# Optimization experiments

Hardware: AMD Instinct MI355X
Metric: run time of the kernel (lower is better)

## Reference

```python
import jax, jax.numpy as jnp
import numpy as np

EXP = 2          # self.exp
NEG = -1e9       # mask fill value
B, N1, DIM, F = 4, 1024, 1024, 4
N = N1 + 1
NTOT = F * N     # 4100


def _normalize(x):
    # L2-normalize along last dim; also return the norm (keepdims)
    n = jnp.sqrt(jnp.sum(x * x, axis=-1, keepdims=True))
    return x / n, n


def setup_inputs() -> dict:
    key = jax.random.key(0)
    k1, k2 = jax.random.split(key)
    lhs = jax.random.normal(k1, (B, N1, DIM), dtype=jnp.float32)
    rhs = jax.random.normal(k2, (B, NTOT, DIM), dtype=jnp.float32)
    return {"lhs": lhs, "rhs": rhs}


def reference(lhs, rhs):
    b, n1, dim = lhs.shape
    n = n1 + 1
    ntot = rhs.shape[1]
    f = ntot // n

    lhs_n, lhs_norm = _normalize(lhs)          # (B,N1,D), (B,N1,1)
    rhs_n, _ = _normalize(rhs)                 # (B,Ntot,D)

    # cosine similarity GEMM + power epilogue
    sim = jnp.einsum('bnd,bmd->bnm', lhs_n, rhs_n) ** EXP   # (B,N1,Ntot)

    # view as (B, N1, F, N); torch masks:
    #   sim4[..., -N1:][~eye] = -1e9   (off-diagonal of last N1 cols)
    #   sim4[..., 0] = -1e9            (first col of each frame)
    # net keep condition: j == i + 1
    sim4 = sim.reshape(b, n1, f, n)
    i = jnp.arange(n1)[:, None, None]   # (N1,1,1)
    j = jnp.arange(n)[None, None, :]    # (1,1,N)
    keep = (j == i + 1)                 # (N1,1,N), broadcasts over F
    sim4 = jnp.where(keep, sim4, jnp.float32(NEG))

    return sim4.reshape(b, n1, ntot), lhs_norm
```

## Files before the change

### kernel.cpp

```cpp
#include <hip/hip_runtime.h>

#define BB   4
#define N1   1024
#define DIM  1024
#define FF   4
#define NN   1025
#define NTOT (FF * NN)
#define SIM_TOTAL ((size_t)BB * N1 * NTOT)
#define NEGV (-1e9f)

typedef float f4 __attribute__((ext_vector_type(4)));

__device__ __forceinline__ f4 nt_load(const f4* p)  { return __builtin_nontemporal_load(p); }
__device__ __forceinline__ void nt_store(f4* p, f4 v) { __builtin_nontemporal_store(v, p); }

__global__ __launch_bounds__(256)
void lcs_kernel(const float* __restrict__ lhs,
                const float* __restrict__ rhs,
                float* __restrict__ out) {
    const int lane = threadIdx.x & 63;
    const int row  = (blockIdx.x << 2) | (threadIdx.x >> 6);
    const int b    = row >> 10;
    const int i    = row & (N1 - 1);

    f4* orow4 = (f4*)(out + (size_t)row * NTOT);
    const f4 negv = { NEGV, NEGV, NEGV, NEGV };
#pragma unroll
    for (int c = 0; c < 16; ++c)
        nt_store(orow4 + lane + 64 * c, negv);
    if (lane == 0)
        nt_store(orow4 + 1024, negv);

    const f4* lrow = (const f4*)(lhs + (size_t)row * DIM);
    f4 lv[4];
#pragma unroll
    for (int c = 0; c < 4; ++c)
        lv[c] = nt_load(lrow + lane + 64 * c);

    float l2 = 0.f;
#pragma unroll
    for (int c = 0; c < 4; ++c)
        l2 += lv[c].x * lv[c].x + lv[c].y * lv[c].y
            + lv[c].z * lv[c].z + lv[c].w * lv[c].w;

    float dot[FF], r2[FF];
#pragma unroll
    for (int f = 0; f < FF; ++f) {
        const size_t rrow_idx = (size_t)b * NTOT + (size_t)f * NN + (i + 1);
        const f4* rrow = (const f4*)(rhs + rrow_idx * DIM);
        float d = 0.f, r = 0.f;
#pragma unroll
        for (int c = 0; c < 4; ++c) {
            const f4 rv = nt_load(rrow + lane + 64 * c);
            d += lv[c].x * rv.x + lv[c].y * rv.y + lv[c].z * rv.z + lv[c].w * rv.w;
            r += rv.x * rv.x + rv.y * rv.y + rv.z * rv.z + rv.w * rv.w;
        }
        dot[f] = d;
        r2[f]  = r;
    }

    float vals[9];
    vals[0] = l2;
#pragma unroll
    for (int f = 0; f < FF; ++f) {
        vals[1 + 2 * f] = dot[f];
        vals[2 + 2 * f] = r2[f];
    }
#pragma unroll
    for (int q = 0; q < 9; ++q) {
#pragma unroll
        for (int off = 32; off > 0; off >>= 1)
            vals[q] += __shfl_xor(vals[q], off, 64);
    }

    asm volatile("s_waitcnt vmcnt(0)" ::: "memory");
    if (lane == 0) {
        const float l2s = vals[0];
        float* orow = out + (size_t)row * NTOT;
#pragma unroll
        for (int f = 0; f < FF; ++f) {
            const float d = vals[1 + 2 * f];
            const float r = vals[2 + 2 * f];
            orow[f * NN + i + 1] = (d * d) / (l2s * r);
        }
        out[SIM_TOTAL + row] = sqrtf(l2s);
    }
}

extern "C" void kernel_launch(void* const* d_in, const int* in_sizes, int n_in,
                              void* d_out, int out_size, void* d_ws, size_t ws_size,
                              hipStream_t stream) {
    const float* lhs = (const float*)d_in[0];
    const float* rhs = (const float*)d_in[1];
    float* out = (float*)d_out;

    lcs_kernel<<<BB * N1 / 4, 256, 0, stream>>>(lhs, rhs, out);
}
```

Baseline: 129.3 us.

## Process two rows per wave, prefetch all inputs, and write masked float4s directly

Each wave now handles two rows. All lhs and rhs vectors for both rows are loaded up front to raise memory-level parallelism. The -1e9 fill skips the float4 slots that hold diagonal values; the lane owning each such slot writes a full float4 that mixes the sim value with fill. This removes the scalar overwrite and its ordering wait. Nontemporal load/store hints are dropped, and launch bounds request 2 blocks per CU, which risks register pressure from the large prefetch arrays.

Result: no change. 129.0 us (-0.2%).

```diff
diff --git a/kernel.cpp b/kernel.cpp
--- a/kernel.cpp
+++ b/kernel.cpp
@@ -11,79 +11,114 @@
 
 typedef float f4 __attribute__((ext_vector_type(4)));
 
-__device__ __forceinline__ f4 nt_load(const f4* p)  { return __builtin_nontemporal_load(p); }
-__device__ __forceinline__ void nt_store(f4* p, f4 v) { __builtin_nontemporal_store(v, p); }
-
-__global__ __launch_bounds__(256)
+__global__ __launch_bounds__(256, 2)
 void lcs_kernel(const float* __restrict__ lhs,
                 const float* __restrict__ rhs,
                 float* __restrict__ out) {
     const int lane = threadIdx.x & 63;
-    const int row  = (blockIdx.x << 2) | (threadIdx.x >> 6);
-    const int b    = row >> 10;
-    const int i    = row & (N1 - 1);
+    const int w    = (blockIdx.x << 2) | (threadIdx.x >> 6);
 
-    f4* orow4 = (f4*)(out + (size_t)row * NTOT);
+    int rows[2];
+    rows[0] = w;
+    rows[1] = w + 2048;
+
+    f4 lv[2][4];
+    f4 rv[2][FF][4];
+#pragma unroll
+    for (int t = 0; t < 2; ++t) {
+        const int row = rows[t];
+        const int b   = row >> 10;
+        const int i   = row & (N1 - 1);
+        const f4* lrow = (const f4*)(lhs + (size_t)row * DIM);
+#pragma unroll
+        for (int c = 0; c < 4; ++c)
+            lv[t][c] = lrow[lane + 64 * c];
+#pragma unroll
+        for (int f = 0; f < FF; ++f) {
+            const f4* rrow =
+                (const f4*)(rhs + ((size_t)b * NTOT + (size_t)f * NN + (i + 1)) * DIM);
+#pragma unroll
+            for (int c = 0; c < 4; ++c)
+                rv[t][f][c] = rrow[lane + 64 * c];
+        }
+    }
+
+    int kf[2][FF], mf[2][FF];
+    unsigned smask[2];
+#pragma unroll
+    for (int t = 0; t < 2; ++t) {
+        const int i = rows[t] & (N1 - 1);
+        unsigned m = 0;
+#pragma unroll
+        for (int f = 0; f < FF; ++f) {
+            const int j = f * NN + i + 1;
+            kf[t][f] = j >> 2;
+            mf[t][f] = j & 3;
+            if ((kf[t][f] & 63) == lane)
+                m |= 1u << (kf[t][f] >> 6);
+        }
+        smask[t] = m;
+    }
+
     const f4 negv = { NEGV, NEGV, NEGV, NEGV };
 #pragma unroll
-    for (int c = 0; c < 16; ++c)
-        nt_store(orow4 + lane + 64 * c, negv);
-    if (lane == 0)
-        nt_store(orow4 + 1024, negv);
-
-    const f4* lrow = (const f4*)(lhs + (size_t)row * DIM);
-    f4 lv[4];
+    for (int t = 0; t < 2; ++t) {
+        f4* orow4 = (f4*)(out + (size_t)rows[t] * NTOT);
 #pragma unroll
-    for (int c = 0; c < 4; ++c)
-        lv[c] = nt_load(lrow + lane + 64 * c);
-
-    float l2 = 0.f;
-#pragma unroll
-    for (int c = 0; c < 4; ++c)
-        l2 += lv[c].x * lv[c].x + lv[c].y * lv[c].y
-            + lv[c].z * lv[c].z + lv[c].w * lv[c].w;
-
-    float dot[FF], r2[FF];
-#pragma unroll
-    for (int f = 0; f < FF; ++f) {
-        const size_t rrow_idx = (size_t)b * NTOT + (size_t)f * NN + (i + 1);
-        const f4* rrow = (const f4*)(rhs + rrow_idx * DIM);
-        float d = 0.f, r = 0.f;
-#pragma unroll
-        for (int c = 0; c < 4; ++c) {
-            const f4 rv = nt_load(rrow + lane + 64 * c);
-            d += lv[c].x * rv.x + lv[c].y * rv.y + lv[c].z * rv.z + lv[c].w * rv.w;
-            r += rv.x * rv.x + rv.y * rv.y + rv.z * rv.z + rv.w * rv.w;
-        }
-        dot[f] = d;
-        r2[f]  = r;
+        for (int c = 0; c < 16; ++c)
+            if (!((smask[t] >> c) & 1))
+                orow4[lane + 64 * c] = negv;
+        if (lane == 0 && !((smask[t] >> 16) & 1))
+            orow4[1024] = negv;
     }
 
-    float vals[9];
-    vals[0] = l2;
 #pragma unroll
-    for (int f = 0; f < FF; ++f) {
-        vals[1 + 2 * f] = dot[f];
-        vals[2 + 2 * f] = r2[f];
-    }
+    for (int t = 0; t < 2; ++t) {
+        float vals[9];
+        float l2 = 0.f;
 #pragma unroll
-    for (int q = 0; q < 9; ++q) {
-#pragma unroll
-        for (int off = 32; off > 0; off >>= 1)
-            vals[q] += __shfl_xor(vals[q], off, 64);
-    }
-
-    asm volatile("s_waitcnt vmcnt(0)" ::: "memory");
-    if (lane == 0) {
-        const float l2s = vals[0];
-        float* orow = out + (size_t)row * NTOT;
+        for (int c = 0; c < 4; ++c)
+            l2 += lv[t][c].x * lv[t][c].x + lv[t][c].y * lv[t][c].y
+                + lv[t][c].z * lv[t][c].z + lv[t][c].w * lv[t][c].w;
+        vals[0] = l2;
 #pragma unroll
         for (int f = 0; f < FF; ++f) {
-            const float d = vals[1 + 2 * f];
-            const float r = vals[2 + 2 * f];
-            orow[f * NN + i + 1] = (d * d) / (l2s * r);
+            float d = 0.f, r = 0.f;
+#pragma unroll
+            for (int c = 0; c < 4; ++c) {
+                const f4 a = lv[t][c], bz = rv[t][f][c];
+                d += a.x * bz.x + a.y * bz.y + a.z * bz.z + a.w * bz.w;
+                r += bz.x * bz.x + bz.y * bz.y + bz.z * bz.z + bz.w * bz.w;
+            }
+            vals[1 + 2 * f] = d;
+            vals[2 + 2 * f] = r;
         }
-        out[SIM_TOTAL + row] = sqrtf(l2s);
+
+#pragma unroll
+        for (int q = 0; q < 9; ++q) {
+#pragma unroll
+            for (int off = 32; off > 0; off >>= 1)
+                vals[q] += __shfl_xor(vals[q], off, 64);
+        }
+
+        const float l2s = vals[0];
+        f4* orow4 = (f4*)(out + (size_t)rows[t] * NTOT);
+#pragma unroll
+        for (int f = 0; f < FF; ++f) {
+            if ((kf[t][f] & 63) == lane) {
+                const float d   = vals[1 + 2 * f];
+                const float r   = vals[2 + 2 * f];
+                const float sim = (d * d) / (l2s * r);
+                f4 v;
+                v.x = (mf[t][f] == 0) ? sim : NEGV;
+                v.y = (mf[t][f] == 1) ? sim : NEGV;
+                v.z = (mf[t][f] == 2) ? sim : NEGV;
+                v.w = (mf[t][f] == 3) ? sim : NEGV;
+                orow4[kf[t][f]] = v;
+            }
+        }
+        if (lane == 0)
+            out[SIM_TOTAL + rows[t]] = sqrtf(l2s);
     }
 }
 
@@ -94,5 +129,5 @@
     const float* rhs = (const float*)d_in[1];
     float* out = (float*)d_out;
 
-    lcs_kernel<<<BB * N1 / 4, 256, 0, stream>>>(lhs, rhs, out);
+    lcs_kernel<<<512, 256, 0, stream>>>(lhs, rhs, out);
 }
```

## Hoist all input loads, skip overwritten fill stores, drop nontemporal hints

Applied to the files above, without the earlier changes.

Issues all lhs and rhs vector loads up front so they are in flight together, before the -1e9 fill stores. Each lane works out which float4 slots hold a diagonal similarity value, skips the fill store for those slots, and later writes the full float4 with the sim value merged in. This removes the duplicate store and the vmcnt(0) wait. Nontemporal load/store builtins are replaced with ordinary accesses, which changes cache behaviour for a write-heavy kernel, and holding the prefetched rhs rows raises register use.

New measurement: 126.3 us. 1.02x faster.

```diff
diff --git a/kernel.cpp b/kernel.cpp
--- a/kernel.cpp
+++ b/kernel.cpp
@@ -11,9 +11,6 @@
 
 typedef float f4 __attribute__((ext_vector_type(4)));
 
-__device__ __forceinline__ f4 nt_load(const f4* p)  { return __builtin_nontemporal_load(p); }
-__device__ __forceinline__ void nt_store(f4* p, f4 v) { __builtin_nontemporal_store(v, p); }
-
 __global__ __launch_bounds__(256)
 void lcs_kernel(const float* __restrict__ lhs,
                 const float* __restrict__ rhs,
@@ -23,49 +20,64 @@
     const int b    = row >> 10;
     const int i    = row & (N1 - 1);
 
+    const f4* lrow = (const f4*)(lhs + (size_t)row * DIM);
+    f4 lv[4];
+#pragma unroll
+    for (int c = 0; c < 4; ++c)
+        lv[c] = lrow[lane + 64 * c];
+
+    f4 rv[FF][4];
+#pragma unroll
+    for (int f = 0; f < FF; ++f) {
+        const f4* rrow =
+            (const f4*)(rhs + ((size_t)b * NTOT + (size_t)f * NN + (i + 1)) * DIM);
+#pragma unroll
+        for (int c = 0; c < 4; ++c)
+            rv[f][c] = rrow[lane + 64 * c];
+    }
+
+    int kf[FF], mf[FF];
+    unsigned smask = 0;
+#pragma unroll
+    for (int f = 0; f < FF; ++f) {
+        const int j = f * NN + i + 1;
+        kf[f] = j >> 2;
+        mf[f] = j & 3;
+        if ((kf[f] & 63) == lane)
+            smask |= 1u << (kf[f] >> 6);
+    }
+
     f4* orow4 = (f4*)(out + (size_t)row * NTOT);
     const f4 negv = { NEGV, NEGV, NEGV, NEGV };
 #pragma unroll
     for (int c = 0; c < 16; ++c)
-        nt_store(orow4 + lane + 64 * c, negv);
-    if (lane == 0)
-        nt_store(orow4 + 1024, negv);
+        if (!((smask >> c) & 1))
+            orow4[lane + 64 * c] = negv;
+    if (lane == 0 && !((smask >> 16) & 1))
+        orow4[1024] = negv;
 
-    const f4* lrow = (const f4*)(lhs + (size_t)row * DIM);
-    f4 lv[4];
+    float vals[9];
+    {
+        float l2 = 0.f;
 #pragma unroll
-    for (int c = 0; c < 4; ++c)
-        lv[c] = nt_load(lrow + lane + 64 * c);
-
-    float l2 = 0.f;
-#pragma unroll
-    for (int c = 0; c < 4; ++c)
-        l2 += lv[c].x * lv[c].x + lv[c].y * lv[c].y
-            + lv[c].z * lv[c].z + lv[c].w * lv[c].w;
-
-    float dot[FF], r2[FF];
+        for (int c = 0; c < 4; ++c)
+            l2 += lv[c].x * lv[c].x + lv[c].y * lv[c].y
+                + lv[c].z * lv[c].z + lv[c].w * lv[c].w;
+        vals[0] = l2;
+    }
 #pragma unroll
     for (int f = 0; f < FF; ++f) {
-        const size_t rrow_idx = (size_t)b * NTOT + (size_t)f * NN + (i + 1);
-        const f4* rrow = (const f4*)(rhs + rrow_idx * DIM);
         float d = 0.f, r = 0.f;
 #pragma unroll
         for (int c = 0; c < 4; ++c) {
-            const f4 rv = nt_load(rrow + lane + 64 * c);
-            d += lv[c].x * rv.x + lv[c].y * rv.y + lv[c].z * rv.z + lv[c].w * rv.w;
-            r += rv.x * rv.x + rv.y * rv.y + rv.z * rv.z + rv.w * rv.w;
+            const f4 a = lv[c], z = rv[f][c];
+            d += a.x * z.x + a.y * z.y + a.z * z.z + a.w * z.w;
+            r += z.x * z.x + z.y * z.y + z.z * z.z + z.w * z.w;
         }
-        dot[f] = d;
-        r2[f]  = r;
+        vals[1 + 2 * f] = d;
+        vals[2 + 2 * f] = r;
     }
 
-    float vals[9];
-    vals[0] = l2;
-#pragma unroll
-    for (int f = 0; f < FF; ++f) {
-        vals[1 + 2 * f] = dot[f];
-        vals[2 + 2 * f] = r2[f];
-    }
 #pragma unroll
     for (int q = 0; q < 9; ++q) {
 #pragma unroll
@@ -73,18 +85,23 @@
             vals[q] += __shfl_xor(vals[q], off, 64);
     }
 
-    asm volatile("s_waitcnt vmcnt(0)" ::: "memory");
-    if (lane == 0) {
-        const float l2s = vals[0];
-        float* orow = out + (size_t)row * NTOT;
+    const float l2s = vals[0];
 #pragma unroll
-        for (int f = 0; f < FF; ++f) {
-            const float d = vals[1 + 2 * f];
-            const float r = vals[2 + 2 * f];
-            orow[f * NN + i + 1] = (d * d) / (l2s * r);
+    for (int f = 0; f < FF; ++f) {
+        if ((kf[f] & 63) == lane) {
+            const float d   = vals[1 + 2 * f];
+            const float r   = vals[2 + 2 * f];
+            const float sim = (d * d) / (l2s * r);
+            f4 v;
+            v.x = (mf[f] == 0) ? sim : NEGV;
+            v.y = (mf[f] == 1) ? sim : NEGV;
+            v.z = (mf[f] == 2) ? sim : NEGV;
+            v.w = (mf[f] == 3) ? sim : NEGV;
+            orow4[kf[f]] = v;
         }
+    }
+    if (lane == 0)
         out[SIM_TOTAL + row] = sqrtf(l2s);
-    }
 }
 
 extern "C" void kernel_launch(void* const* d_in, const int* in_sizes, int n_in,
```
